# Optimization experiments

Measured on AMD Instinct MI355X. Metric: run time of the kernel, lower is better.

The kernel has to match this reference:

```python
import jax, jax.numpy as jnp
import numpy as np

N = 200000   # nodes
E = 6400000  # edges (avg degree 32)
T = 6        # member feature dim
M = 10       # fingerprint dim
L = 4        # R + 1 layers
GIN = 14     # group_level_input
GLO = 10     # group_level_output


def setup_inputs() -> dict:
    key = jax.random.key(0)
    ks = jax.random.split(key, 10)
    return {
        "x_member": jax.random.normal(ks[0], (N, T), dtype=jnp.float32),
        "x_group": jax.random.normal(ks[1], (1, GIN), dtype=jnp.float32),
        "src": jax.random.randint(ks[2], (E,), 0, N, dtype=jnp.int32),
        "dst": jax.random.randint(ks[3], (E,), 0, N, dtype=jnp.int32),
        "H": jax.random.normal(ks[4], (L, T, M), dtype=jnp.float32),
        "W": jax.random.normal(ks[5], (L,), dtype=jnp.float32),
        "gW": jax.random.normal(ks[6], (GLO, GIN), dtype=jnp.float32) * 0.1,
        "gb": jax.random.normal(ks[7], (GLO,), dtype=jnp.float32),
        "mW": jax.random.normal(ks[8], (3, M + GLO), dtype=jnp.float32) * 0.1,
        "mb": jax.random.normal(ks[9], (3,), dtype=jnp.float32),
    }


def reference(x_member, x_group, src, dst, H, W, gW, gb, mW, mb):
    n = x_member.shape[0]
    # message passing: neighbor feature sum per destination node  [N, T]
    neigh = jax.ops.segment_sum(x_member[src], dst, num_segments=n)
    v1 = x_member + neigh  # r[a] + sum of neighbor r's; r is layer-invariant
    # all R+1 layers at once: [L, N, M]
    v2 = jax.nn.sigmoid(jnp.einsum("nt,ltm->lnm", v1, H))
    fl = jax.nn.softmax(v2 * W[:, None, None], axis=-1)
    # f starts at zeros and accumulates softmax over every node and layer -> [1, M]
    f = jnp.sum(fl, axis=(0, 1))[None, :]
    # group-level perceptron
    g = jax.nn.sigmoid(x_group @ gW.T + gb)  # [1, GLO]
    merged = jnp.concatenate([f, g], axis=1)  # [1, M+GLO]
    return jax.nn.softmax(merged @ mW.T + mb, axis=-1)  # [1, 3]
```

## Files before the change

kernel.cpp:

```cpp
#include <hip/hip_runtime.h>
#include <hip/hip_fp16.h>
#include <math.h>

#define TDIM 6
#define MDIM 10
#define LDIM 4
#define GIND 14
#define GLOD 10

#define BINSHIFT 8
#define BINSZ 256
#define MAXBINS 1024

#define SC2_BLOCKS 512
#define SC2_THREADS 512
#define SC2_CHQ 1408
#define SC2_CHUNKS 3
#define SC2_TQ 3
#define OVF_ENT 16384
#define META2 2048

#define SC_BLOCK 512
#define SC_EPT 32
#define SC_EPB (SC_BLOCK * SC_EPT)
#define AC_BLOCK 512
#define AC_CAP 8704
#define AC_EPT 17

__global__ void zero32_k(unsigned* __restrict__ p, int n) {
    int i = blockIdx.x * blockDim.x + threadIdx.x;
    if (i < n) p[i] = 0u;
}

__device__ __forceinline__ void add_row4(uint4 r, float& s0, float& s1, float& s2,
                                         float& s3, float& s4, float& s5) {
    float2 a0 = __half22float2(*(__half2*)&r.x);
    float2 a1 = __half22float2(*(__half2*)&r.y);
    float2 a2 = __half22float2(*(__half2*)&r.z);
    s0 += a0.x; s1 += a0.y; s2 += a1.x; s3 += a1.y; s4 += a2.x; s5 += a2.y;
}


__global__ __launch_bounds__(SC2_THREADS) void scat2_k(
        const float* __restrict__ xm, int N, uint4* __restrict__ xh,
        const int* __restrict__ src, const int* __restrict__ dst, int E, int NQ, int QPB,
        unsigned* __restrict__ gcount, unsigned* __restrict__ ebuf, int C, int nbins,
        uint2* __restrict__ ovf, unsigned* __restrict__ ocur) {
    __shared__ unsigned lcount[MAXBINS];
    __shared__ unsigned lbase[MAXBINS];
    __shared__ unsigned lcur[MAXBINS];
    __shared__ unsigned cstart[MAXBINS];
    __shared__ unsigned wsum[8];
    __shared__ unsigned spk[SC2_CHQ * 4];
    __shared__ unsigned sgp[SC2_CHQ * 4];
    int tid = threadIdx.x;
    for (int i = tid; i < MAXBINS; i += SC2_THREADS) { lcount[i] = 0u; lcur[i] = 0u; }

    int gid = blockIdx.x * SC2_THREADS + tid;
    int gstride = gridDim.x * SC2_THREADS;
    for (int n = gid; n < N; n += gstride) {
        const float2* r = (const float2*)(xm + (size_t)n * TDIM);
        float2 a = r[0], b = r[1], c = r[2];
        __half2 h0 = __floats2half2_rn(a.x, a.y);
        __half2 h1 = __floats2half2_rn(b.x, b.y);
        __half2 h2 = __floats2half2_rn(c.x, c.y);
        uint4 o;
        o.x = *(unsigned*)&h0; o.y = *(unsigned*)&h1; o.z = *(unsigned*)&h2; o.w = 0u;
        xh[n] = o;
    }
    if (blockIdx.x == 0) {
        for (int e = NQ * 4 + tid; e < E; e += SC2_THREADS) {
            unsigned oc = atomicAdd(ocur, 1u);
            if (oc < OVF_ENT) ovf[oc] = make_uint2((unsigned)src[e], (unsigned)dst[e]);
        }
    }
    __syncthreads();

    int qb = blockIdx.x * QPB;
    int qend = qb + QPB; if (qend > NQ) qend = NQ;
    const int4* s4p = (const int4*)src;
    const int4* d4p = (const int4*)dst;

    for (int q = qb + tid; q < qend; q += SC2_THREADS) {
        int4 dv = d4p[q];
        atomicAdd(&lcount[((unsigned)dv.x) >> BINSHIFT], 1u);
        atomicAdd(&lcount[((unsigned)dv.y) >> BINSHIFT], 1u);
        atomicAdd(&lcount[((unsigned)dv.z) >> BINSHIFT], 1u);
        atomicAdd(&lcount[((unsigned)dv.w) >> BINSHIFT], 1u);
    }
    __syncthreads();
    for (int i = tid; i < nbins; i += SC2_THREADS) {
        unsigned c = lcount[i];
        if (c) lbase[i] = atomicAdd(&gcount[i], c);
    }
    __syncthreads();

    for (int ch = 0; ch < SC2_CHUNKS; ch++) {
        int cb = qb + ch * SC2_CHQ;
        if (cb >= qend) break;
        int ce = cb + SC2_CHQ; if (ce > qend) ce = qend;
        for (int i = tid; i < MAXBINS; i += SC2_THREADS) lcount[i] = 0u;
        __syncthreads();

        unsigned pk[SC2_TQ * 4];
        unsigned wr[SC2_TQ * 4];
#pragma unroll
        for (int i = 0; i < SC2_TQ; i++) {
            int q = cb + tid + i * SC2_THREADS;
            if (q < ce) {
                int4 sv = s4p[q];
                int4 dv = d4p[q];
                {
                    unsigned du = (unsigned)dv.x, b = du >> BINSHIFT;
                    pk[i*4+0] = ((du & (BINSZ-1)) << 18) | (unsigned)sv.x;
                    wr[i*4+0] = (b << 18) | atomicAdd(&lcount[b], 1u);
                }
                {
                    unsigned du = (unsigned)dv.y, b = du >> BINSHIFT;
                    pk[i*4+1] = ((du & (BINSZ-1)) << 18) | (unsigned)sv.y;
                    wr[i*4+1] = (b << 18) | atomicAdd(&lcount[b], 1u);
                }
                {
                    unsigned du = (unsigned)dv.z, b = du >> BINSHIFT;
                    pk[i*4+2] = ((du & (BINSZ-1)) << 18) | (unsigned)sv.z;
                    wr[i*4+2] = (b << 18) | atomicAdd(&lcount[b], 1u);
                }
                {
                    unsigned du = (unsigned)dv.w, b = du >> BINSHIFT;
                    pk[i*4+3] = ((du & (BINSZ-1)) << 18) | (unsigned)sv.w;
                    wr[i*4+3] = (b << 18) | atomicAdd(&lcount[b], 1u);
                }
            } else {
                pk[i*4+0] = 0xFFFFFFFFu; pk[i*4+1] = 0xFFFFFFFFu;
                pk[i*4+2] = 0xFFFFFFFFu; pk[i*4+3] = 0xFFFFFFFFu;
            }
        }
        __syncthreads();

        unsigned a0 = lcount[2*tid], a1 = lcount[2*tid+1];
        {
            unsigned s = a0 + a1;
            int lane = tid & 63;
#pragma unroll
            for (int off = 1; off < 64; off <<= 1) {
                unsigned t = (unsigned)__shfl_up((int)s, off, 64);
                if (lane >= off) s += t;
            }
            if (lane == 63) wsum[tid >> 6] = s;
            __syncthreads();
            unsigned add = 0; int w = tid >> 6;
#pragma unroll
            for (int ww = 0; ww < 7; ww++) if (ww < w) add += wsum[ww];
            unsigned excl = s + add - (a0 + a1);
            cstart[2*tid] = excl;
            cstart[2*tid+1] = excl + a0;
        }
        __syncthreads();

#pragma unroll
        for (int k = 0; k < SC2_TQ * 4; k++) {
            unsigned p = pk[k];
            if (p != 0xFFFFFFFFu) {
                unsigned b = wr[k] >> 18;
                unsigned r = wr[k] & 0x3FFFFu;
                unsigned li = cstart[b] + r;
                unsigned pos = lbase[b] + lcur[b] + r;
                if (pos < (unsigned)C) {
                    spk[li] = p;
                    sgp[li] = b * (unsigned)C + pos;
                } else {
                    spk[li] = 0xFFFFFFFFu;
                    unsigned oc = atomicAdd(ocur, 1u);
                    if (oc < OVF_ENT) {
                        ovf[oc] = make_uint2(p & 0x3FFFFu,
                                             (b << BINSHIFT) | (p >> 18));
                    }
                }
            }
        }
        __syncthreads();

        unsigned T = cstart[MAXBINS-1] + lcount[MAXBINS-1];
        for (unsigned j = tid; j < T; j += SC2_THREADS) {
            unsigned p = spk[j];
            if (p != 0xFFFFFFFFu) ebuf[sgp[j]] = p;
        }
        lcur[2*tid]   += a0;
        lcur[2*tid+1] += a1;
        __syncthreads();
    }
}

__global__ __launch_bounds__(AC_BLOCK) void accum2_k(
        const float* __restrict__ xm, const uint4* __restrict__ xh,
        const unsigned* __restrict__ ebuf, const unsigned* __restrict__ gcount, int C,
        const unsigned* __restrict__ ocur, const uint2* __restrict__ ovf,
        const float* __restrict__ H, const float* __restrict__ W,
        float* __restrict__ facc, int N) {
    __shared__ unsigned srt[AC_CAP];
    __shared__ unsigned cnt[BINSZ];
    __shared__ unsigned cstart[BINSZ];
    __shared__ unsigned wsum[8];
    __shared__ unsigned ovl[256];
    __shared__ unsigned ovn;
    __shared__ float sH[LDIM * TDIM * MDIM];
    __shared__ float sW[LDIM];
    __shared__ float sred[AC_BLOCK / 64][MDIM];
    float (*part)[BINSZ][TDIM] = (float(*)[BINSZ][TDIM])srt;
    int tid = threadIdx.x;
    int bin = blockIdx.x;
    for (int i = tid; i < LDIM * TDIM * MDIM; i += AC_BLOCK) sH[i] = H[i];
    if (tid < LDIM) sW[tid] = W[tid];
    if (tid < BINSZ) cnt[tid] = 0u;
    if (tid == 0) ovn = 0u;
    __syncthreads();

    unsigned gc = gcount[bin];
    unsigned m = gc < (unsigned)C ? gc : (unsigned)C;
    unsigned e0 = (unsigned)bin * (unsigned)C;
    int nbase = bin << BINSHIFT;

    unsigned ed_[AC_EPT];
    unsigned rk_[AC_EPT];
#pragma unroll
    for (int k = 0; k < AC_EPT; k++) {
        unsigned i = (unsigned)tid + (unsigned)k * AC_BLOCK;
        if (i < m) {
            unsigned v = __builtin_nontemporal_load(ebuf + e0 + i);
            ed_[k] = v;
            rk_[k] = atomicAdd(&cnt[v >> 18], 1u);
        }
    }
    {
        unsigned novf = *ocur;
        if (novf > OVF_ENT) novf = OVF_ENT;
        for (unsigned i = tid; i < novf; i += AC_BLOCK) {
            uint2 e = ovf[i];
            if ((e.y >> BINSHIFT) == (unsigned)bin) {
                unsigned u = atomicAdd(&ovn, 1u);
                if (u < 256u) ovl[u] = ((e.y & (BINSZ-1)) << 18) | e.x;
            }
        }
    }
    __syncthreads();

    {
        unsigned v = (tid < BINSZ) ? cnt[tid] : 0u;
        int lane = tid & 63;
#pragma unroll
        for (int off = 1; off < 64; off <<= 1) {
            unsigned t = (unsigned)__shfl_up((int)v, off, 64);
            if (lane >= off) v += t;
        }
        if (tid < BINSZ && lane == 63) wsum[tid >> 6] = v;
        __syncthreads();
        if (tid < BINSZ) {
            unsigned add = 0;
            int w = tid >> 6;
#pragma unroll
            for (int ww = 0; ww < 3; ww++) if (ww < w) add += wsum[ww];
            cstart[tid] = v + add - cnt[tid];
        }
        __syncthreads();
    }

#pragma unroll
    for (int k = 0; k < AC_EPT; k++) {
        unsigned i = (unsigned)tid + (unsigned)k * AC_BLOCK;
        if (i < m) {
            unsigned v = ed_[k];
            srt[cstart[v >> 18] + rk_[k]] = v & 0x3FFFFu;
        }
    }
    __syncthreads();

    int node = tid & (BINSZ - 1);
    int role = tid >> 8;
    int n = nbase + node;
    float s0 = 0.f, s1 = 0.f, s2 = 0.f, s3 = 0.f, s4 = 0.f, s5 = 0.f;
    if (n < N) {
        unsigned c = cnt[node];
        unsigned b0 = cstart[node];
        unsigned h = c >> 1;
        unsigned j  = role ? h : 0u;
        unsigned je = role ? c : h;
        for (; j + 8 <= je; j += 8) {
            unsigned i0 = srt[b0 + j],     i1 = srt[b0 + j + 1];
            unsigned i2 = srt[b0 + j + 2], i3 = srt[b0 + j + 3];
            unsigned i4 = srt[b0 + j + 4], i5 = srt[b0 + j + 5];
            unsigned i6 = srt[b0 + j + 6], i7 = srt[b0 + j + 7];
            uint4 r0 = xh[i0], r1 = xh[i1], r2 = xh[i2], r3 = xh[i3];
            uint4 r4 = xh[i4], r5 = xh[i5], r6 = xh[i6], r7 = xh[i7];
            add_row4(r0, s0, s1, s2, s3, s4, s5);
            add_row4(r1, s0, s1, s2, s3, s4, s5);
            add_row4(r2, s0, s1, s2, s3, s4, s5);
            add_row4(r3, s0, s1, s2, s3, s4, s5);
            add_row4(r4, s0, s1, s2, s3, s4, s5);
            add_row4(r5, s0, s1, s2, s3, s4, s5);
            add_row4(r6, s0, s1, s2, s3, s4, s5);
            add_row4(r7, s0, s1, s2, s3, s4, s5);
        }
        for (; j + 2 <= je; j += 2) {
            unsigned ia = srt[b0 + j], ib = srt[b0 + j + 1];
            uint4 ra = xh[ia], rb = xh[ib];
            add_row4(ra, s0, s1, s2, s3, s4, s5);
            add_row4(rb, s0, s1, s2, s3, s4, s5);
        }
        if (j < je) {
            uint4 ra = xh[srt[b0 + j]];
            add_row4(ra, s0, s1, s2, s3, s4, s5);
        }
        if (role == 0) {
            unsigned no = ovn < 256u ? ovn : 256u;
            for (unsigned q = 0; q < no; q++) {
                unsigned o = ovl[q];
                if ((int)(o >> 18) == node) {
                    uint4 rr = xh[o & 0x3FFFFu];
                    add_row4(rr, s0, s1, s2, s3, s4, s5);
                }
            }
        }
    }
    __syncthreads();
    part[role][node][0] = s0; part[role][node][1] = s1; part[role][node][2] = s2;
    part[role][node][3] = s3; part[role][node][4] = s4; part[role][node][5] = s5;
    __syncthreads();

    float fs[MDIM];
#pragma unroll
    for (int mm = 0; mm < MDIM; mm++) fs[mm] = 0.f;

    if (n < N) {
        float v[TDIM];
        const float2* xr = (const float2*)(xm + (size_t)n * TDIM);
        float2 x0 = xr[0], x1 = xr[1], x2 = xr[2];
        v[0] = x0.x + part[0][node][0] + part[1][node][0];
        v[1] = x0.y + part[0][node][1] + part[1][node][1];
        v[2] = x1.x + part[0][node][2] + part[1][node][2];
        v[3] = x1.y + part[0][node][3] + part[1][node][3];
        v[4] = x2.x + part[0][node][4] + part[1][node][4];
        v[5] = x2.y + part[0][node][5] + part[1][node][5];

        int lb = role << 1;
#pragma unroll
        for (int li = 0; li < 2; li++) {
            int l = lb + li;
            float z[MDIM];
#pragma unroll
            for (int mm = 0; mm < MDIM; mm++) {
                float a2 = 0.f;
#pragma unroll
                for (int t = 0; t < TDIM; t++) a2 += v[t] * sH[(l * TDIM + t) * MDIM + mm];
                z[mm] = a2;
            }
            float wl = sW[l];
            float mx = -1e30f;
#pragma unroll
            for (int mm = 0; mm < MDIM; mm++) {
                float sg = wl / (1.f + __expf(-z[mm]));
                z[mm] = sg;
                mx = fmaxf(mx, sg);
            }
            float se = 0.f;
#pragma unroll
            for (int mm = 0; mm < MDIM; mm++) {
                float e = __expf(z[mm] - mx);
                z[mm] = e;
                se += e;
            }
            float inv = 1.f / se;
#pragma unroll
            for (int mm = 0; mm < MDIM; mm++) fs[mm] += z[mm] * inv;
        }
    }

#pragma unroll
    for (int mm = 0; mm < MDIM; mm++) {
        float v = fs[mm];
#pragma unroll
        for (int off = 32; off > 0; off >>= 1) v += __shfl_down(v, off, 64);
        fs[mm] = v;
    }
    int wave = tid >> 6, lane = tid & 63;
    if (lane == 0) {
#pragma unroll
        for (int mm = 0; mm < MDIM; mm++) sred[wave][mm] = fs[mm];
    }
    __syncthreads();
    if (tid < MDIM) {
        float s = 0.f;
#pragma unroll
        for (int w = 0; w < AC_BLOCK / 64; w++) s += sred[w][tid];
        atomicAdd(facc + tid, s);
    }
}


__global__ __launch_bounds__(256) void prep_k(const float* __restrict__ xm, int N,
                                              uint4* __restrict__ xh,
                                              const int* __restrict__ dst, int E,
                                              unsigned* __restrict__ hist, int nbins) {
    __shared__ unsigned lh[MAXBINS];
    for (int i = threadIdx.x; i < MAXBINS; i += blockDim.x) lh[i] = 0u;
    __syncthreads();
    int gid = blockIdx.x * blockDim.x + threadIdx.x;
    int gstride = gridDim.x * blockDim.x;
    for (int n = gid; n < N; n += gstride) {
        const float2* r = (const float2*)(xm + (size_t)n * TDIM);
        float2 a = r[0], b = r[1], c = r[2];
        __half2 h0 = __floats2half2_rn(a.x, a.y);
        __half2 h1 = __floats2half2_rn(b.x, b.y);
        __half2 h2 = __floats2half2_rn(c.x, c.y);
        uint4 o;
        o.x = *(unsigned*)&h0; o.y = *(unsigned*)&h1; o.z = *(unsigned*)&h2; o.w = 0u;
        xh[n] = o;
    }
    int e4 = E >> 2;
    const int4* d4p = (const int4*)dst;
    for (int i = gid; i < e4; i += gstride) {
        int4 d = d4p[i];
        atomicAdd(&lh[((unsigned)d.x) >> BINSHIFT], 1u);
        atomicAdd(&lh[((unsigned)d.y) >> BINSHIFT], 1u);
        atomicAdd(&lh[((unsigned)d.z) >> BINSHIFT], 1u);
        atomicAdd(&lh[((unsigned)d.w) >> BINSHIFT], 1u);
    }
    for (int e = (e4 << 2) + gid; e < E; e += gstride)
        atomicAdd(&lh[((unsigned)dst[e]) >> BINSHIFT], 1u);
    __syncthreads();
    for (int i = threadIdx.x; i < nbins; i += blockDim.x)
        if (lh[i]) atomicAdd(&hist[i], lh[i]);
}

__global__ __launch_bounds__(MAXBINS) void scan_k(const unsigned* __restrict__ hist,
                                                  unsigned* __restrict__ offsets,
                                                  unsigned* __restrict__ gfill, int nbins) {
    __shared__ unsigned buf[2][MAXBINS];
    int t = threadIdx.x;
    buf[0][t] = (t < nbins) ? hist[t] : 0u;
    __syncthreads();
    int cur = 0;
    for (int off = 1; off < MAXBINS; off <<= 1) {
        unsigned v = buf[cur][t];
        if (t >= off) v += buf[cur][t - off];
        buf[cur ^ 1][t] = v;
        __syncthreads();
        cur ^= 1;
    }
    if (t < nbins) {
        unsigned ex = t ? buf[cur][t - 1] : 0u;
        offsets[t] = ex;
        gfill[t] = ex;
    }
    if (t == 0) offsets[nbins] = buf[cur][nbins - 1];
}

__global__ __launch_bounds__(SC_BLOCK) void scatter_k(const int* __restrict__ src,
                                                      const int* __restrict__ dst, int E,
                                                      unsigned* __restrict__ gfill,
                                                      unsigned* __restrict__ ebuf, int nbins) {
    __shared__ unsigned lcount[MAXBINS];
    __shared__ unsigned lbase[MAXBINS];
    for (int i = threadIdx.x; i < MAXBINS; i += SC_BLOCK) lcount[i] = 0u;
    __syncthreads();
    int base = blockIdx.x * SC_EPB + threadIdx.x * SC_EPT;
    int s[SC_EPT], d[SC_EPT];
    unsigned rk[SC_EPT];
#pragma unroll
    for (int q = 0; q < SC_EPT / 4; q++) {
        int e = base + q * 4;
        if (e + 3 < E) {
            int4 s4 = *(const int4*)(src + e);
            int4 d4 = *(const int4*)(dst + e);
            s[q*4+0] = s4.x; s[q*4+1] = s4.y; s[q*4+2] = s4.z; s[q*4+3] = s4.w;
            d[q*4+0] = d4.x; d[q*4+1] = d4.y; d[q*4+2] = d4.z; d[q*4+3] = d4.w;
        } else {
#pragma unroll
            for (int k = 0; k < 4; k++) {
                int ee = e + k;
                s[q*4+k] = (ee < E) ? src[ee] : -1;
                d[q*4+k] = (ee < E) ? dst[ee] : 0;
            }
        }
    }
#pragma unroll
    for (int k = 0; k < SC_EPT; k++)
        if (s[k] >= 0) rk[k] = atomicAdd(&lcount[((unsigned)d[k]) >> BINSHIFT], 1u);
    __syncthreads();
    for (int i = threadIdx.x; i < nbins; i += SC_BLOCK) {
        unsigned c = lcount[i];
        if (c) lbase[i] = atomicAdd(&gfill[i], c);
    }
    __syncthreads();
#pragma unroll
    for (int k = 0; k < SC_EPT; k++) {
        if (s[k] >= 0) {
            unsigned du = (unsigned)d[k];
            unsigned b = du >> BINSHIFT;
            unsigned pack = ((du & (BINSZ - 1)) << 18) | (unsigned)s[k];
            ebuf[lbase[b] + rk[k]] = pack;
        }
    }
}

__global__ __launch_bounds__(AC_BLOCK) void accum_node_k(
        const float* __restrict__ xm, const uint4* __restrict__ xh,
        const unsigned* __restrict__ ebuf, const unsigned* __restrict__ offsets,
        const float* __restrict__ H, const float* __restrict__ W,
        float* __restrict__ facc, int N) {
    __shared__ unsigned srt[AC_CAP];
    __shared__ unsigned cnt[BINSZ];
    __shared__ unsigned tmp[BINSZ];
    __shared__ unsigned cstart[BINSZ];
    __shared__ float sH[LDIM * TDIM * MDIM];
    __shared__ float sW[LDIM];
    __shared__ float sred[AC_BLOCK / 64][MDIM];
    int tid = threadIdx.x;
    int bin = blockIdx.x;
    for (int i = tid; i < LDIM * TDIM * MDIM; i += AC_BLOCK) sH[i] = H[i];
    if (tid < LDIM) sW[tid] = W[tid];
    if (tid < BINSZ) cnt[tid] = 0u;
    __syncthreads();

    unsigned e0 = offsets[bin], e1 = offsets[bin + 1];
    unsigned total = e1 - e0;
    unsigned m = total < AC_CAP ? total : AC_CAP;
    int nbase = bin << BINSHIFT;

    unsigned ed_[AC_EPT];
    unsigned rk_[AC_EPT];
#pragma unroll
    for (int k = 0; k < AC_EPT; k++) {
        unsigned idx = e0 + (unsigned)tid + (unsigned)k * AC_BLOCK;
        if (idx < e0 + m) {
            unsigned v = ebuf[idx];
            ed_[k] = v;
            rk_[k] = atomicAdd(&cnt[v >> 18], 1u);
        }
    }
    __syncthreads();

    if (tid < BINSZ) tmp[tid] = cnt[tid];
    __syncthreads();
    for (int off = 1; off < BINSZ; off <<= 1) {
        unsigned v = 0;
        if (tid < BINSZ) { v = tmp[tid]; if (tid >= off) v += tmp[tid - off]; }
        __syncthreads();
        if (tid < BINSZ) tmp[tid] = v;
        __syncthreads();
    }
    if (tid < BINSZ) cstart[tid] = tmp[tid] - cnt[tid];
    __syncthreads();

#pragma unroll
    for (int k = 0; k < AC_EPT; k++) {
        unsigned idx = e0 + (unsigned)tid + (unsigned)k * AC_BLOCK;
        if (idx < e0 + m) {
            unsigned v = ed_[k];
            srt[cstart[v >> 18] + rk_[k]] = v & 0x3FFFFu;
        }
    }
    __syncthreads();

    float fs[MDIM];
#pragma unroll
    for (int mm = 0; mm < MDIM; mm++) fs[mm] = 0.f;

    int n = nbase + tid;
    if (tid < BINSZ && n < N) {
        float s0 = 0.f, s1 = 0.f, s2 = 0.f, s3 = 0.f, s4 = 0.f, s5 = 0.f;
        unsigned c = cnt[tid];
        unsigned b0 = cstart[tid];
        unsigned j = 0;
        for (; j + 2 <= c; j += 2) {
            unsigned sa = srt[b0 + j], sb = srt[b0 + j + 1];
            uint4 ra = xh[sa];
            uint4 rb = xh[sb];
            add_row4(ra, s0, s1, s2, s3, s4, s5);
            add_row4(rb, s0, s1, s2, s3, s4, s5);
        }
        if (j < c) {
            uint4 ra = xh[srt[b0 + j]];
            add_row4(ra, s0, s1, s2, s3, s4, s5);
        }
        for (unsigned idx = e0 + m; idx < e1; idx++) {
            unsigned v = ebuf[idx];
            if ((int)(v >> 18) == tid) {
                uint4 ra = xh[v & 0x3FFFFu];
                add_row4(ra, s0, s1, s2, s3, s4, s5);
            }
        }

        float v[TDIM];
        const float2* xr = (const float2*)(xm + (size_t)n * TDIM);
        float2 x0 = xr[0], x1 = xr[1], x2 = xr[2];
        v[0] = x0.x + s0; v[1] = x0.y + s1;
        v[2] = x1.x + s2; v[3] = x1.y + s3;
        v[4] = x2.x + s4; v[5] = x2.y + s5;

#pragma unroll
        for (int l = 0; l < LDIM; l++) {
            float z[MDIM];
#pragma unroll
            for (int mm = 0; mm < MDIM; mm++) {
                float a2 = 0.f;
#pragma unroll
                for (int t = 0; t < TDIM; t++) a2 += v[t] * sH[(l * TDIM + t) * MDIM + mm];
                z[mm] = a2;
            }
            float wl = sW[l];
            float mx = -1e30f;
#pragma unroll
            for (int mm = 0; mm < MDIM; mm++) {
                float sg = wl / (1.f + __expf(-z[mm]));
                z[mm] = sg;
                mx = fmaxf(mx, sg);
            }
            float se = 0.f;
#pragma unroll
            for (int mm = 0; mm < MDIM; mm++) {
                float e = __expf(z[mm] - mx);
                z[mm] = e;
                se += e;
            }
            float inv = 1.f / se;
#pragma unroll
            for (int mm = 0; mm < MDIM; mm++) fs[mm] += z[mm] * inv;
        }
    }

#pragma unroll
    for (int mm = 0; mm < MDIM; mm++) {
        float v = fs[mm];
#pragma unroll
        for (int off = 32; off > 0; off >>= 1) v += __shfl_down(v, off, 64);
        fs[mm] = v;
    }
    int wave = tid >> 6, lane = tid & 63;
    if (lane == 0) {
#pragma unroll
        for (int mm = 0; mm < MDIM; mm++) sred[wave][mm] = fs[mm];
    }
    __syncthreads();
    if (tid < MDIM) {
        float s = 0.f;
#pragma unroll
        for (int w = 0; w < AC_BLOCK / 64; w++) s += sred[w][tid];
        atomicAdd(facc + tid, s);
    }
}

__global__ void finalize_k(const float* __restrict__ facc,
                           const float* __restrict__ xg,
                           const float* __restrict__ gW,
                           const float* __restrict__ gb,
                           const float* __restrict__ mW,
                           const float* __restrict__ mb,
                           float* __restrict__ out) {
    if (threadIdx.x == 0 && blockIdx.x == 0) {
        float merged[MDIM + GLOD];
#pragma unroll
        for (int m = 0; m < MDIM; m++) merged[m] = facc[m];
        for (int j = 0; j < GLOD; j++) {
            float a = gb[j];
            for (int i = 0; i < GIND; i++) a += xg[i] * gW[j * GIND + i];
            merged[MDIM + j] = 1.f / (1.f + __expf(-a));
        }
        float lg[3];
        float mx = -1e30f;
        for (int k = 0; k < 3; k++) {
            float a = mb[k];
            for (int j = 0; j < MDIM + GLOD; j++) a += merged[j] * mW[k * (MDIM + GLOD) + j];
            lg[k] = a;
            mx = fmaxf(mx, a);
        }
        float se = 0.f;
        for (int k = 0; k < 3; k++) { lg[k] = __expf(lg[k] - mx); se += lg[k]; }
        float inv = 1.f / se;
        for (int k = 0; k < 3; k++) out[k] = lg[k] * inv;
    }
}

__global__ void fb_zero_k(float* __restrict__ ws, int n) {
    int i = blockIdx.x * blockDim.x + threadIdx.x;
    if (i < n) ws[i] = 0.f;
}

__global__ void fb_edge_scatter_k(const float* __restrict__ xm,
                                  const int* __restrict__ src,
                                  const int* __restrict__ dst,
                                  float* __restrict__ neigh, int E) {
    int e = blockIdx.x * blockDim.x + threadIdx.x;
    if (e >= E) return;
    int s = src[e], d = dst[e];
    const float2* r = (const float2*)(xm + (size_t)s * TDIM);
    float2 a = r[0], b = r[1], c = r[2];
    float* o = neigh + (size_t)d * TDIM;
    atomicAdd(o + 0, a.x); atomicAdd(o + 1, a.y);
    atomicAdd(o + 2, b.x); atomicAdd(o + 3, b.y);
    atomicAdd(o + 4, c.x); atomicAdd(o + 5, c.y);
}

__global__ __launch_bounds__(256) void fb_node_k(
        const float* __restrict__ xm, const float* __restrict__ neigh,
        const float* __restrict__ H, const float* __restrict__ W,
        float* __restrict__ facc, int N) {
    __shared__ float sH[LDIM * TDIM * MDIM];
    __shared__ float sW[LDIM];
    __shared__ float sred[4][MDIM];
    int tid = threadIdx.x;
    for (int i = tid; i < LDIM * TDIM * MDIM; i += blockDim.x) sH[i] = H[i];
    if (tid < LDIM) sW[tid] = W[tid];
    __syncthreads();
    float fs[MDIM];
#pragma unroll
    for (int m = 0; m < MDIM; m++) fs[m] = 0.f;
    for (int n = blockIdx.x * blockDim.x + tid; n < N; n += gridDim.x * blockDim.x) {
        float v[TDIM];
        const float2* xr = (const float2*)(xm + (size_t)n * TDIM);
        const float2* nr = (const float2*)(neigh + (size_t)n * TDIM);
#pragma unroll
        for (int t2 = 0; t2 < 3; t2++) {
            float2 a = xr[t2], b = nr[t2];
            v[2 * t2 + 0] = a.x + b.x;
            v[2 * t2 + 1] = a.y + b.y;
        }
#pragma unroll
        for (int l = 0; l < LDIM; l++) {
            float z[MDIM];
#pragma unroll
            for (int m = 0; m < MDIM; m++) {
                float a2 = 0.f;
#pragma unroll
                for (int t = 0; t < TDIM; t++) a2 += v[t] * sH[(l * TDIM + t) * MDIM + m];
                z[m] = a2;
            }
            float wl = sW[l], mx = -1e30f;
#pragma unroll
            for (int m = 0; m < MDIM; m++) { float sg = wl / (1.f + __expf(-z[m])); z[m] = sg; mx = fmaxf(mx, sg); }
            float se = 0.f;
#pragma unroll
            for (int m = 0; m < MDIM; m++) { float e = __expf(z[m] - mx); z[m] = e; se += e; }
            float inv = 1.f / se;
#pragma unroll
            for (int m = 0; m < MDIM; m++) fs[m] += z[m] * inv;
        }
    }
#pragma unroll
    for (int m = 0; m < MDIM; m++) {
        float v = fs[m];
#pragma unroll
        for (int off = 32; off > 0; off >>= 1) v += __shfl_down(v, off, 64);
        fs[m] = v;
    }
    int wave = tid >> 6, lane = tid & 63;
    if (lane == 0) {
#pragma unroll
        for (int m = 0; m < MDIM; m++) sred[wave][m] = fs[m];
    }
    __syncthreads();
    if (tid < MDIM) {
        float s = sred[0][tid] + sred[1][tid] + sred[2][tid] + sred[3][tid];
        atomicAdd(facc + tid, s);
    }
}

extern "C" void kernel_launch(void* const* d_in, const int* in_sizes, int n_in,
                              void* d_out, int out_size, void* d_ws, size_t ws_size,
                              hipStream_t stream) {
    const float* xm  = (const float*)d_in[0];
    const float* xg  = (const float*)d_in[1];
    const int*   src = (const int*)d_in[2];
    const int*   dst = (const int*)d_in[3];
    const float* H   = (const float*)d_in[4];
    const float* W   = (const float*)d_in[5];
    const float* gW  = (const float*)d_in[6];
    const float* gb  = (const float*)d_in[7];
    const float* mW  = (const float*)d_in[8];
    const float* mb  = (const float*)d_in[9];
    float* out = (float*)d_out;

    int N = in_sizes[0] / TDIM;
    int E = in_sizes[2];
    int nbins = (N + BINSZ - 1) >> BINSHIFT;
    size_t ws_words = ws_size / 4;
    size_t xh_words = (size_t)N * 4;

    long fixed = (long)(xh_words + META2 + (size_t)OVF_ENT * 2);
    long avail = (long)ws_words - fixed;
    long C = avail > 0 ? (avail / nbins) & ~3L : 0;
    if (C > AC_CAP) C = AC_CAP;
    double mu = (double)E / nbins;
    long Cmin = (long)(mu + 4.0 * sqrt(mu) + 32.0);
    int NQ = E >> 2;
    int QPB = (NQ + SC2_BLOCKS - 1) / SC2_BLOCKS;
    bool ok1 = (C >= Cmin) && nbins <= MAXBINS && N <= (1 << 18) &&
               QPB <= SC2_CHUNKS * SC2_CHQ;

    size_t meta_words2 = MAXBINS + (MAXBINS + 1) + MAXBINS + 16;
    size_t need2 = (xh_words + (size_t)E + meta_words2) * 4;
    bool ok2 = ws_size >= need2 && nbins <= MAXBINS && N <= (1 << 18);

    if (ok1) {
        uint4*    xh     = (uint4*)d_ws;
        unsigned* ebuf   = (unsigned*)d_ws + xh_words;
        unsigned* gcount = ebuf + (size_t)nbins * C;
        unsigned* ocur   = gcount + MAXBINS;
        float*    facc   = (float*)(ocur + 16);
        uint2*    ovf    = (uint2*)(gcount + META2);

        zero32_k<<<(META2 + 255) / 256, 256, 0, stream>>>(gcount, META2);
        scat2_k<<<SC2_BLOCKS, SC2_THREADS, 0, stream>>>(xm, N, xh, src, dst, E, NQ, QPB,
                                                        gcount, ebuf, (int)C, nbins, ovf, ocur);
        accum2_k<<<nbins, AC_BLOCK, 0, stream>>>(xm, xh, ebuf, gcount, (int)C, ocur, ovf,
                                                 H, W, facc, N);
        finalize_k<<<1, 64, 0, stream>>>(facc, xg, gW, gb, mW, mb, out);
    } else if (ok2) {
        uint4*    xh      = (uint4*)d_ws;
        unsigned* ebuf    = (unsigned*)d_ws + xh_words;
        unsigned* hist    = ebuf + (size_t)E;
        unsigned* offsets = hist + MAXBINS;
        unsigned* gfill   = offsets + MAXBINS + 1;
        float*    facc    = (float*)(gfill + MAXBINS);

        zero32_k<<<(int)((meta_words2 + 255) / 256), 256, 0, stream>>>(hist, (int)meta_words2);
        prep_k<<<1024, 256, 0, stream>>>(xm, N, xh, dst, E, hist, nbins);
        scan_k<<<1, MAXBINS, 0, stream>>>(hist, offsets, gfill, nbins);
        scatter_k<<<(E + SC_EPB - 1) / SC_EPB, SC_BLOCK, 0, stream>>>(src, dst, E, gfill, ebuf, nbins);
        accum_node_k<<<nbins, AC_BLOCK, 0, stream>>>(xm, xh, ebuf, offsets, H, W, facc, N);
        finalize_k<<<1, 64, 0, stream>>>(facc, xg, gW, gb, mW, mb, out);
    } else {
        float* neigh = (float*)d_ws;
        float* facc  = neigh + (size_t)N * TDIM;
        int zn = N * TDIM + 16;
        fb_zero_k<<<(zn + 255) / 256, 256, 0, stream>>>(neigh, zn);
        fb_edge_scatter_k<<<(E + 255) / 256, 256, 0, stream>>>(xm, src, dst, neigh, E);
        fb_node_k<<<256, 256, 0, stream>>>(xm, neigh, H, W, facc, N);
        finalize_k<<<1, 64, 0, stream>>>(facc, xg, gW, gb, mW, mb, out);
    }
}
```

Before: 114.3 us.

## Split per-bin accumulation into two half-bin blocks plus separate epilogue kernel

Replaces the single accum2_k with two kernels. accum_a_k processes each bin with two blocks, each handling half of the bin's edges and using half the shared memory. Each block writes partial per-node sums to a global buffer. accum_b_k then combines the two partials with x and computes the sigmoid/softmax fingerprint. The aim is to double block count and raise occupancy for the gather phase, at the cost of an extra kernel launch and a round trip of about 1.2M floats through global memory.

```diff
diff --git a/kernel.cpp b/kernel.cpp
--- a/kernel.cpp
+++ b/kernel.cpp
@@ -26,6 +26,10 @@
 #define AC_BLOCK 512
 #define AC_CAP 8704
 #define AC_EPT 17
+
+#define SRT_HALF 4352
+#define AH_EPT 9
+#define PB_NODE (BINSZ * TDIM)
 
 __global__ void zero32_k(unsigned* __restrict__ p, int n) {
     int i = blockIdx.x * blockDim.x + threadIdx.x;
@@ -191,6 +195,226 @@
     }
 }
 
+__global__ __launch_bounds__(512) void accum_a_k(
+        const uint4* __restrict__ xh,
+        const unsigned* __restrict__ ebuf, const unsigned* __restrict__ gcount, int C,
+        const unsigned* __restrict__ ocur, const uint2* __restrict__ ovf,
+        float* __restrict__ pbuf, int nbins) {
+    __shared__ unsigned srt[SRT_HALF];
+    __shared__ unsigned cnt[BINSZ];
+    __shared__ unsigned cstart[BINSZ];
+    __shared__ unsigned wsum[4];
+    __shared__ unsigned ovl[256];
+    __shared__ unsigned ovn;
+    float (*part)[BINSZ][TDIM] = (float(*)[BINSZ][TDIM])srt;
+    int tid = threadIdx.x;
+    int bh = blockIdx.x;
+    int bin = bh >> 1;
+    unsigned half = (unsigned)(bh & 1);
+    if (tid < BINSZ) cnt[tid] = 0u;
+    if (tid == 0) ovn = 0u;
+    __syncthreads();
+
+    unsigned gc = gcount[bin];
+    unsigned m = gc < (unsigned)C ? gc : (unsigned)C;
+    unsigned lo = half ? (m >> 1) : 0u;
+    unsigned hi = half ? m : (m >> 1);
+    unsigned e0 = (unsigned)bin * (unsigned)C;
+
+    unsigned ed_[AH_EPT];
+    unsigned rk_[AH_EPT];
+#pragma unroll
+    for (int k = 0; k < AH_EPT; k++) {
+        ed_[k] = 0xFFFFFFFFu;
+        unsigned i = lo + (unsigned)tid + (unsigned)k * 512u;
+        if (i < hi) {
+            unsigned v = __builtin_nontemporal_load(ebuf + e0 + i);
+            ed_[k] = v;
+            rk_[k] = atomicAdd(&cnt[v >> 18], 1u);
+        }
+    }
+    if (half == 0u) {
+        unsigned novf = *ocur;
+        if (novf > OVF_ENT) novf = OVF_ENT;
+        for (unsigned i = tid; i < novf; i += 512u) {
+            uint2 e = ovf[i];
+            if ((e.y >> BINSHIFT) == (unsigned)bin) {
+                unsigned u = atomicAdd(&ovn, 1u);
+                if (u < 256u) ovl[u] = ((e.y & (BINSZ-1)) << 18) | e.x;
+            }
+        }
+    }
+    __syncthreads();
+
+    {
+        unsigned v = (tid < BINSZ) ? cnt[tid] : 0u;
+        int lane = tid & 63;
+#pragma unroll
+        for (int off = 1; off < 64; off <<= 1) {
+            unsigned t = (unsigned)__shfl_up((int)v, off, 64);
+            if (lane >= off) v += t;
+        }
+        if (tid < BINSZ && lane == 63) wsum[tid >> 6] = v;
+        __syncthreads();
+        if (tid < BINSZ) {
+            unsigned add = 0;
+            int w = tid >> 6;
+#pragma unroll
+            for (int ww = 0; ww < 3; ww++) if (ww < w) add += wsum[ww];
+            cstart[tid] = v + add - cnt[tid];
+        }
+        __syncthreads();
+    }
+
+#pragma unroll
+    for (int k = 0; k < AH_EPT; k++) {
+        unsigned v = ed_[k];
+        if (v != 0xFFFFFFFFu) srt[cstart[v >> 18] + rk_[k]] = v & 0x3FFFFu;
+    }
+    __syncthreads();
+
+    int node = tid & (BINSZ - 1);
+    int role = tid >> 8;
+    float s0 = 0.f, s1 = 0.f, s2 = 0.f, s3 = 0.f, s4 = 0.f, s5 = 0.f;
+    {
+        unsigned c = cnt[node];
+        unsigned b0 = cstart[node];
+        unsigned h2 = c >> 1;
+        unsigned j  = role ? h2 : 0u;
+        unsigned je = role ? c : h2;
+        for (; j + 8 <= je; j += 8) {
+            unsigned i0 = srt[b0 + j],     i1 = srt[b0 + j + 1];
+            unsigned i2 = srt[b0 + j + 2], i3 = srt[b0 + j + 3];
+            unsigned i4 = srt[b0 + j + 4], i5 = srt[b0 + j + 5];
+            unsigned i6 = srt[b0 + j + 6], i7 = srt[b0 + j + 7];
+            uint4 r0 = xh[i0], r1 = xh[i1], r2 = xh[i2], r3 = xh[i3];
+            uint4 r4 = xh[i4], r5 = xh[i5], r6 = xh[i6], r7 = xh[i7];
+            add_row4(r0, s0, s1, s2, s3, s4, s5);
+            add_row4(r1, s0, s1, s2, s3, s4, s5);
+            add_row4(r2, s0, s1, s2, s3, s4, s5);
+            add_row4(r3, s0, s1, s2, s3, s4, s5);
+            add_row4(r4, s0, s1, s2, s3, s4, s5);
+            add_row4(r5, s0, s1, s2, s3, s4, s5);
+            add_row4(r6, s0, s1, s2, s3, s4, s5);
+            add_row4(r7, s0, s1, s2, s3, s4, s5);
+        }
+        for (; j + 2 <= je; j += 2) {
+            unsigned ia = srt[b0 + j], ib = srt[b0 + j + 1];
+            uint4 ra = xh[ia], rb = xh[ib];
+            add_row4(ra, s0, s1, s2, s3, s4, s5);
+            add_row4(rb, s0, s1, s2, s3, s4, s5);
+        }
+        if (j < je) {
+            uint4 ra = xh[srt[b0 + j]];
+            add_row4(ra, s0, s1, s2, s3, s4, s5);
+        }
+        if (role == 0) {
+            unsigned no = ovn < 256u ? ovn : 256u;
+            for (unsigned q = 0; q < no; q++) {
+                unsigned o = ovl[q];
+                if ((int)(o >> 18) == node) {
+                    uint4 rr = xh[o & 0x3FFFFu];
+                    add_row4(rr, s0, s1, s2, s3, s4, s5);
+                }
+            }
+        }
+    }
+    __syncthreads();
+    part[role][node][0] = s0; part[role][node][1] = s1; part[role][node][2] = s2;
+    part[role][node][3] = s3; part[role][node][4] = s4; part[role][node][5] = s5;
+    __syncthreads();
+
+    float* pb = pbuf + (size_t)bh * PB_NODE;
+    for (int j = tid; j < PB_NODE; j += 512) {
+        int nd = j / TDIM, d = j - nd * TDIM;
+        pb[j] = part[0][nd][d] + part[1][nd][d];
+    }
+}
+
+__global__ __launch_bounds__(256) void accum_b_k(
+        const float* __restrict__ xm, const float* __restrict__ pbuf,
+        const float* __restrict__ H, const float* __restrict__ W,
+        float* __restrict__ facc, int N) {
+    __shared__ float sH[LDIM * TDIM * MDIM];
+    __shared__ float sW[LDIM];
+    __shared__ float sred[4][MDIM];
+    int tid = threadIdx.x;
+    for (int i = tid; i < LDIM * TDIM * MDIM; i += 256) sH[i] = H[i];
+    if (tid < LDIM) sW[tid] = W[tid];
+    __syncthreads();
+
+    int n = blockIdx.x * 256 + tid;
+    float fs[MDIM];
+#pragma unroll
+    for (int mm = 0; mm < MDIM; mm++) fs[mm] = 0.f;
+
+    if (n < N) {
+        int bin = n >> BINSHIFT;
+        int node = n & (BINSZ - 1);
+        const float* p0 = pbuf + (size_t)(bin * 2 + 0) * PB_NODE + node * TDIM;
+        const float* p1 = pbuf + (size_t)(bin * 2 + 1) * PB_NODE + node * TDIM;
+        const float2* xr = (const float2*)(xm + (size_t)n * TDIM);
+        float2 x0 = xr[0], x1 = xr[1], x2 = xr[2];
+        float v[TDIM];
+        v[0] = x0.x + p0[0] + p1[0];
+        v[1] = x0.y + p0[1] + p1[1];
+        v[2] = x1.x + p0[2] + p1[2];
+        v[3] = x1.y + p0[3] + p1[3];
+        v[4] = x2.x + p0[4] + p1[4];
+        v[5] = x2.y + p0[5] + p1[5];
+
+#pragma unroll
+        for (int l = 0; l < LDIM; l++) {
+            float z[MDIM];
+#pragma unroll
+            for (int mm = 0; mm < MDIM; mm++) {
+                float a2 = 0.f;
+#pragma unroll
+                for (int t = 0; t < TDIM; t++) a2 += v[t] * sH[(l * TDIM + t) * MDIM + mm];
+                z[mm] = a2;
+            }
+            float wl = sW[l];
+            float mx = -1e30f;
+#pragma unroll
+            for (int mm = 0; mm < MDIM; mm++) {
+                float sg = wl / (1.f + __expf(-z[mm]));
+                z[mm] = sg;
+                mx = fmaxf(mx, sg);
+            }
+            float se = 0.f;
+#pragma unroll
+            for (int mm = 0; mm < MDIM; mm++) {
+                float e = __expf(z[mm] - mx);
+                z[mm] = e;
+                se += e;
+            }
+            float inv = 1.f / se;
+#pragma unroll
+            for (int mm = 0; mm < MDIM; mm++) fs[mm] += z[mm] * inv;
+        }
+    }
+
+#pragma unroll
+    for (int mm = 0; mm < MDIM; mm++) {
+        float v = fs[mm];
+#pragma unroll
+        for (int off = 32; off > 0; off >>= 1) v += __shfl_down(v, off, 64);
+        fs[mm] = v;
+    }
+    int wave = tid >> 6, lane = tid & 63;
+    if (lane == 0) {
+#pragma unroll
+        for (int mm = 0; mm < MDIM; mm++) sred[wave][mm] = fs[mm];
+    }
+    __syncthreads();
+    if (tid < MDIM) {
+        float s = 0.f;
+#pragma unroll
+        for (int w = 0; w < 4; w++) s += sred[w][tid];
+        atomicAdd(facc + tid, s);
+    }
+}
+
 __global__ __launch_bounds__(AC_BLOCK) void accum2_k(
         const float* __restrict__ xm, const uint4* __restrict__ xh,
         const unsigned* __restrict__ ebuf, const unsigned* __restrict__ gcount, int C,
@@ -784,23 +1008,47 @@
     int nbins = (N + BINSZ - 1) >> BINSHIFT;
     size_t ws_words = ws_size / 4;
     size_t xh_words = (size_t)N * 4;
+    size_t pbuf_words = (size_t)nbins * 2 * PB_NODE;
+
+    double mu = (double)E / nbins;
+    long Cmin = (long)(mu + 4.0 * sqrt(mu) + 32.0);
+    int NQ = E >> 2;
+    int QPB = (NQ + SC2_BLOCKS - 1) / SC2_BLOCKS;
+    bool qpb_ok = QPB <= SC2_CHUNKS * SC2_CHQ;
+
+    long fixed_s = (long)(xh_words + META2 + (size_t)OVF_ENT * 2 + pbuf_words);
+    long avail_s = (long)ws_words - fixed_s;
+    long Cs = avail_s > 0 ? (avail_s / nbins) & ~3L : 0;
+    if (Cs > AC_CAP) Cs = AC_CAP;
+    bool ok1s = (Cs >= Cmin) && nbins <= MAXBINS && N <= (1 << 18) && qpb_ok;
 
     long fixed = (long)(xh_words + META2 + (size_t)OVF_ENT * 2);
     long avail = (long)ws_words - fixed;
     long C = avail > 0 ? (avail / nbins) & ~3L : 0;
     if (C > AC_CAP) C = AC_CAP;
-    double mu = (double)E / nbins;
-    long Cmin = (long)(mu + 4.0 * sqrt(mu) + 32.0);
-    int NQ = E >> 2;
-    int QPB = (NQ + SC2_BLOCKS - 1) / SC2_BLOCKS;
-    bool ok1 = (C >= Cmin) && nbins <= MAXBINS && N <= (1 << 18) &&
-               QPB <= SC2_CHUNKS * SC2_CHQ;
+    bool ok1 = (C >= Cmin) && nbins <= MAXBINS && N <= (1 << 18) && qpb_ok;
 
     size_t meta_words2 = MAXBINS + (MAXBINS + 1) + MAXBINS + 16;
     size_t need2 = (xh_words + (size_t)E + meta_words2) * 4;
     bool ok2 = ws_size >= need2 && nbins <= MAXBINS && N <= (1 << 18);
 
-    if (ok1) {
+    if (ok1s) {
+        uint4*    xh     = (uint4*)d_ws;
+        unsigned* ebuf   = (unsigned*)d_ws + xh_words;
+        unsigned* gcount = ebuf + (size_t)nbins * Cs;
+        unsigned* ocur   = gcount + MAXBINS;
+        float*    facc   = (float*)(ocur + 16);
+        uint2*    ovf    = (uint2*)(gcount + META2);
+        float*    pbuf   = (float*)(gcount + META2 + (size_t)OVF_ENT * 2);
+
+        zero32_k<<<(META2 + 255) / 256, 256, 0, stream>>>(gcount, META2);
+        scat2_k<<<SC2_BLOCKS, SC2_THREADS, 0, stream>>>(xm, N, xh, src, dst, E, NQ, QPB,
+                                                        gcount, ebuf, (int)Cs, nbins, ovf, ocur);
+        accum_a_k<<<nbins * 2, 512, 0, stream>>>(xh, ebuf, gcount, (int)Cs, ocur, ovf,
+                                                 pbuf, nbins);
+        accum_b_k<<<(N + 255) / 256, 256, 0, stream>>>(xm, pbuf, H, W, facc, N);
+        finalize_k<<<1, 64, 0, stream>>>(facc, xg, gW, gb, mW, mb, out);
+    } else if (ok1) {
         uint4*    xh     = (uint4*)d_ws;
         unsigned* ebuf   = (unsigned*)d_ws + xh_words;
         unsigned* gcount = ebuf + (size_t)nbins * C;
```

Result: no change. 115.5 us (+1.1%).
